# Kernel tuning notes

Measured on AMD Instinct MI355X. Metric: run time of the kernel, lower is better.

The kernel has to match this reference:

```python
import jax, jax.numpy as jnp
import numpy as np

NUM_EDGE_CLASS = 4
NODE_DIM = 64
BATCH = 8
NUM_NODES = 512


def setup_inputs() -> dict:
    key = jax.random.key(0)
    k1, k2, k3, k4, k5 = jax.random.split(key, 5)
    node_state = jax.random.normal(k1, (BATCH, NUM_NODES, NODE_DIM), dtype=jnp.float32)
    adj_mat = jax.random.randint(k2, (BATCH, NUM_NODES, NUM_NODES), 0, NUM_EDGE_CLASS, dtype=jnp.int32)
    matrix_in = jax.random.normal(k3, (NUM_EDGE_CLASS, NODE_DIM, NODE_DIM), dtype=jnp.float32) * 0.1
    matrix_out = jax.random.normal(k4, (NUM_EDGE_CLASS, NODE_DIM, NODE_DIM), dtype=jnp.float32) * 0.1
    bias = jax.random.normal(k5, (2 * NODE_DIM,), dtype=jnp.float32) * 0.1
    return {"node_state": node_state, "adj_mat": adj_mat,
            "matrix_in": matrix_in, "matrix_out": matrix_out, "bias": bias}


def reference(node_state, adj_mat, matrix_in, matrix_out, bias):
    # Original builds a_in[b,v,w] = matrix_in[adj[b,v,w]] ([B,N,N,D,D]) and a giant
    # [B, N*D, N*D] block matrix; equivalently, with one-hot over edge classes:
    #   msg_in[b,v,d]  = sum_w matrix_in[adj[b,v,w]][d,e]  * h[b,w,e]
    #   msg_out[b,v,d] = sum_w matrix_out[adj[b,w,v]][d,e] * h[b,w,e]  (transposed adj)
    oh = jax.nn.one_hot(adj_mat, matrix_in.shape[0], dtype=node_state.dtype)  # [B,V,W,C]
    msg_in = jnp.einsum('bvwc,cde,bwe->bvd', oh, matrix_in, node_state)
    msg_out = jnp.einsum('bwvc,cde,bwe->bvd', oh, matrix_out, node_state)
    return jnp.concatenate([msg_in, msg_out], axis=-1) + bias  # [B,N,2D]
```

## Files before the change

kernel.cpp:

```cpp
#include <hip/hip_runtime.h>

#define NB 8
#define NN 512
#define DD 64
#define NCLS 4

typedef short bf16x8 __attribute__((ext_vector_type(8)));
typedef float f32x4 __attribute__((ext_vector_type(4)));

__device__ __forceinline__ unsigned short f2bf(float f) {
    unsigned int x = __builtin_bit_cast(unsigned int, f);
    x += 0x7FFFu + ((x >> 16) & 1u);
    return (unsigned short)(x >> 16);
}

__device__ __forceinline__ void gload_lds16(const void* g, void* lds) {
    __builtin_amdgcn_global_load_lds(
        (const __attribute__((address_space(1))) unsigned int*)g,
        (__attribute__((address_space(3))) unsigned int*)lds, 16, 0, 0);
}

__device__ __forceinline__ bf16x8 onehot_packed(unsigned int bits, unsigned int cls) {
    union { unsigned int u[4]; bf16x8 v; } r;
    #pragma unroll
    for (int j = 0; j < 4; ++j) {
        unsigned int c0 = (bits >> (4 * j)) & 3u;
        unsigned int c1 = (bits >> (4 * j + 2)) & 3u;
        r.u[j] = (c0 == cls ? 0x3F80u : 0u) | (c1 == cls ? 0x3F800000u : 0u);
    }
    return r.v;
}

__global__ __launch_bounds__(256) void prep_kernel(
    const float* __restrict__ h, const int* __restrict__ adj,
    const float* __restrict__ Min, const float* __restrict__ Mout,
    unsigned int* __restrict__ packR, unsigned int* __restrict__ packC,
    unsigned short* __restrict__ HTbf, unsigned short* __restrict__ Wbf)
{
    const int blk = blockIdx.x, t = threadIdx.x;
    if (blk < 64) {
        const int b = blk >> 3, r0 = (blk & 7) * 64;
        #pragma unroll
        for (int i = 0; i < 8; ++i) {
            int idx = i * 256 + t;
            int row = r0 + (idx >> 5), pk = idx & 31;
            const int* src = adj + ((size_t)b * NN + row) * NN + pk * 16;
            unsigned int u = 0;
            #pragma unroll
            for (int j = 0; j < 16; ++j) u |= ((unsigned int)src[j] & 3u) << (2 * j);
            packR[((size_t)b * NN + row) * 32 + pk] = u;
        }
    } else if (blk < 576) {
        __shared__ int tile[64][65];
        __shared__ __align__(16) unsigned int tp[64][4];
        const int bb = blk - 64;
        const int b = bb >> 6, tr = ((bb >> 3) & 7) * 64, tc = (bb & 7) * 64;
        const int* src = adj + (size_t)b * NN * NN;
        #pragma unroll
        for (int i = 0; i < 16; ++i) {
            int idx = i * 256 + t, rr = idx >> 6, cc = idx & 63;
            tile[rr][cc] = src[(size_t)(tr + rr) * NN + tc + cc];
        }
        __syncthreads();
        {
            int row = t & 63, part = t >> 6;
            unsigned int u = 0;
            #pragma unroll
            for (int j = 0; j < 16; ++j)
                u |= ((unsigned int)tile[part * 16 + j][row] & 3u) << (2 * j);
            tp[row][part] = u;
        }
        __syncthreads();
        if (t < 64)
            *(uint4*)&packC[((size_t)b * NN + tc + t) * 32 + (tr >> 4)] =
                *(const uint4*)&tp[t][0];
    } else if (blk < 640) {
        const int bb = blk - 576;
        #pragma unroll
        for (int i = 0; i < 16; ++i) {
            int idx = bb * 4096 + i * 256 + t;
            int w = idx & 511, e = (idx >> 9) & 63, b = idx >> 15;
            HTbf[((size_t)b * DD + e) * NN + w] = f2bf(h[((size_t)b * NN + w) * DD + e]);
        }
    } else {
        int idx = (blk - 640) * 256 + t;
        int dir = idx >> 14, d = (idx >> 8) & 63, k = idx & 255;
        int c = k >> 6, e = k & 63;
        const float* M = dir ? Mout : Min;
        Wbf[idx] = f2bf(M[(c * DD + d) * DD + e]);
    }
}

__global__ __launch_bounds__(256) void msg_mfma_kernel(
    const unsigned int* __restrict__ packR, const unsigned int* __restrict__ packC,
    const unsigned short* __restrict__ HTbf, const unsigned short* __restrict__ Wbf,
    const float* __restrict__ bias, float* __restrict__ out)
{
    __shared__ unsigned short HT[2][DD][128];
    __shared__ unsigned short S2[2][8][NCLS * DD];

    const int t = threadIdx.x;
    const int lane = t & 63, wv = t >> 6;
    const int dir = wv >> 1, rt = wv & 1;
    const int b = blockIdx.x >> 6;
    const int v0 = (blockIdx.x & 63) * 8;
    const int r = lane & 15, kb = lane >> 4;

    const unsigned short* HTg = HTbf + (size_t)b * DD * NN;

    auto stage = [&](int s, int c0) {
        #pragma unroll
        for (int q = 0; q < 4; ++q) {
            int L = wv * 4 + q;
            int e = 4 * L + (lane >> 4);
            int off = ((lane & 15) << 4) ^ ((e & 7) << 4);
            const unsigned short* src = HTg + e * NN + c0 * 128 + (off >> 1);
            gload_lds16(src, &HT[s][4 * L][0]);
        }
    };

    stage(0, 0);

    const int vloc = rt * 4 + (r >> 2);
    const unsigned int cls = (unsigned int)(r & 3);
    const unsigned short* prow = (const unsigned short*)(
        (dir ? packC : packR) + ((size_t)b * NN + v0 + vloc) * 32);
    unsigned int bits0  = prow[kb];        unsigned int bits1  = prow[4 + kb];
    unsigned int bits2  = prow[8 + kb];    unsigned int bits3  = prow[12 + kb];
    unsigned int bits4  = prow[16 + kb];   unsigned int bits5  = prow[20 + kb];
    unsigned int bits6  = prow[24 + kb];   unsigned int bits7  = prow[28 + kb];
    unsigned int bits8  = prow[32 + kb];   unsigned int bits9  = prow[36 + kb];
    unsigned int bits10 = prow[40 + kb];   unsigned int bits11 = prow[44 + kb];
    unsigned int bits12 = prow[48 + kb];   unsigned int bits13 = prow[52 + kb];
    unsigned int bits14 = prow[56 + kb];   unsigned int bits15 = prow[60 + kb];

    __syncthreads();

    f32x4 acc[4] = {f32x4{0,0,0,0}, f32x4{0,0,0,0}, f32x4{0,0,0,0}, f32x4{0,0,0,0}};
    #pragma unroll
    for (int c = 0; c < 4; ++c) {
        int s = c & 1;
        if (c < 3) stage(s ^ 1, c + 1);
        #pragma unroll
        for (int kc = 0; kc < 4; ++kc) {
            unsigned int bits;
            switch (c * 4 + kc) {
                case 0:  bits = bits0;  break;  case 1:  bits = bits1;  break;
                case 2:  bits = bits2;  break;  case 3:  bits = bits3;  break;
                case 4:  bits = bits4;  break;  case 5:  bits = bits5;  break;
                case 6:  bits = bits6;  break;  case 7:  bits = bits7;  break;
                case 8:  bits = bits8;  break;  case 9:  bits = bits9;  break;
                case 10: bits = bits10; break;  case 11: bits = bits11; break;
                case 12: bits = bits12; break;  case 13: bits = bits13; break;
                case 14: bits = bits14; break;  default: bits = bits15; break;
            }
            bf16x8 afrag = onehot_packed(bits, cls);
            #pragma unroll
            for (int n = 0; n < 4; ++n) {
                int e = n * 16 + r;
                int boff = (kc * 64 + (kb << 4)) ^ ((e & 7) << 4);
                bf16x8 bfrag = *(const bf16x8*)((const char*)&HT[s][e][0] + boff);
                acc[n] = __builtin_amdgcn_mfma_f32_16x16x32_bf16(afrag, bfrag, acc[n], 0, 0, 0);
            }
        }
        __syncthreads();
    }

    #pragma unroll
    for (int ct = 0; ct < 4; ++ct) {
        #pragma unroll
        for (int rg = 0; rg < 4; ++rg) {
            int row_g = rt * 16 + kb * 4 + rg;
            int vv = row_g >> 2, cc2 = row_g & 3;
            int e = ct * 16 + r;
            int rb = (cc2 * 128 + e * 2) ^ ((vv & 7) << 4);
            *(unsigned short*)((char*)&S2[dir][vv][0] + rb) = f2bf(acc[ct][rg]);
        }
    }
    __syncthreads();

    f32x4 acc2[2] = {f32x4{0,0,0,0}, f32x4{0,0,0,0}};
    #pragma unroll
    for (int kc = 0; kc < 8; ++kc) {
        int vv = r & 7;
        int kbase = kc * 32 + kb * 8;
        int rb = (kbase * 2) ^ (vv << 4);
        bf16x8 a2 = *(const bf16x8*)((const char*)&S2[dir][vv][0] + rb);
        #pragma unroll
        for (int j = 0; j < 2; ++j) {
            int d = (rt * 2 + j) * 16 + r;
            bf16x8 b2 = *(const bf16x8*)&Wbf[(dir * DD + d) * 256 + kbase];
            acc2[j] = __builtin_amdgcn_mfma_f32_16x16x32_bf16(a2, b2, acc2[j], 0, 0, 0);
        }
    }
    #pragma unroll
    for (int j = 0; j < 2; ++j) {
        int d = (rt * 2 + j) * 16 + r;
        float bs = bias[dir * DD + d];
        #pragma unroll
        for (int rg = 0; rg < 4; ++rg) {
            int row = kb * 4 + rg;
            if (row < 8)
                out[((size_t)(b * NN + v0 + row)) * (2 * DD) + dir * DD + d] = acc2[j][rg] + bs;
        }
    }
}

__global__ __launch_bounds__(256) void msg_kernel(
    const float* __restrict__ h, const int* __restrict__ adj,
    const float* __restrict__ Min, const float* __restrict__ Mout,
    const float* __restrict__ bias, float* __restrict__ out)
{
    __shared__ __align__(16) float S[4][2][NCLS][DD];
    const int lane = threadIdx.x & 63, wslot = threadIdx.x >> 6;
    const int wid = blockIdx.x * 4 + wslot;
    const int b = wid >> 9, v = wid & (NN - 1);
    const float* hb = h + (size_t)b * NN * DD;
    const int* adjb = adj + (size_t)b * NN * NN;
    float tot = 0.f, ain1 = 0.f, ain2 = 0.f, ain3 = 0.f, aout1 = 0.f, aout2 = 0.f, aout3 = 0.f;
    for (int w0 = 0; w0 < NN; w0 += 64) {
        int cin_chunk = adjb[v * NN + (w0 + lane)];
        int cout_chunk = adjb[(w0 + lane) * NN + v];
        #pragma unroll
        for (int k = 0; k < 64; ++k) {
            float hw = hb[(w0 + k) * DD + lane];
            int cin = __builtin_amdgcn_readlane(cin_chunk, k);
            int cout = __builtin_amdgcn_readlane(cout_chunk, k);
            tot += hw;
            ain1 = fmaf((cin == 1) ? 1.f : 0.f, hw, ain1);
            ain2 = fmaf((cin == 2) ? 1.f : 0.f, hw, ain2);
            ain3 = fmaf((cin == 3) ? 1.f : 0.f, hw, ain3);
            aout1 = fmaf((cout == 1) ? 1.f : 0.f, hw, aout1);
            aout2 = fmaf((cout == 2) ? 1.f : 0.f, hw, aout2);
            aout3 = fmaf((cout == 3) ? 1.f : 0.f, hw, aout3);
        }
    }
    S[wslot][0][0][lane] = tot - ain1 - ain2 - ain3;
    S[wslot][0][1][lane] = ain1; S[wslot][0][2][lane] = ain2; S[wslot][0][3][lane] = ain3;
    S[wslot][1][0][lane] = tot - aout1 - aout2 - aout3;
    S[wslot][1][1][lane] = aout1; S[wslot][1][2][lane] = aout2; S[wslot][1][3][lane] = aout3;
    __syncthreads();
    float o_in = 0.f, o_out = 0.f;
    #pragma unroll
    for (int c = 0; c < NCLS; ++c)
        for (int e0 = 0; e0 < DD; e0 += 4) {
            float4 mi = *reinterpret_cast<const float4*>(&Min[(c * DD + lane) * DD + e0]);
            float4 mo = *reinterpret_cast<const float4*>(&Mout[(c * DD + lane) * DD + e0]);
            float4 si = *reinterpret_cast<const float4*>(&S[wslot][0][c][e0]);
            float4 so = *reinterpret_cast<const float4*>(&S[wslot][1][c][e0]);
            o_in = fmaf(mi.x, si.x, fmaf(mi.y, si.y, fmaf(mi.z, si.z, fmaf(mi.w, si.w, o_in))));
            o_out = fmaf(mo.x, so.x, fmaf(mo.y, so.y, fmaf(mo.z, so.z, fmaf(mo.w, so.w, o_out))));
        }
    float* ov = out + (size_t)(b * NN + v) * (2 * DD);
    ov[lane] = o_in + bias[lane];
    ov[DD + lane] = o_out + bias[DD + lane];
}

extern "C" void kernel_launch(void* const* d_in, const int* in_sizes, int n_in,
                              void* d_out, int out_size, void* d_ws, size_t ws_size,
                              hipStream_t stream) {
    const float* node_state = (const float*)d_in[0];
    const int*   adj_mat    = (const int*)  d_in[1];
    const float* matrix_in  = (const float*)d_in[2];
    const float* matrix_out = (const float*)d_in[3];
    const float* bias       = (const float*)d_in[4];
    float* out = (float*)d_out;

    const size_t PACKR_OFF = 0;
    const size_t PACKC_OFF = (size_t)NB * NN * 32 * 4;
    const size_t HT_OFF    = PACKC_OFF + (size_t)NB * NN * 32 * 4;
    const size_t W_OFF     = HT_OFF + (size_t)NB * DD * NN * 2;
    const size_t NEED      = W_OFF + (size_t)2 * DD * 256 * 2;

    if (ws_size < NEED) {
        msg_kernel<<<NB * NN / 4, 256, 0, stream>>>(node_state, adj_mat, matrix_in,
                                                    matrix_out, bias, out);
        return;
    }
    unsigned int*   packR = (unsigned int*)((char*)d_ws + PACKR_OFF);
    unsigned int*   packC = (unsigned int*)((char*)d_ws + PACKC_OFF);
    unsigned short* HTbf  = (unsigned short*)((char*)d_ws + HT_OFF);
    unsigned short* Wbf   = (unsigned short*)((char*)d_ws + W_OFF);

    prep_kernel<<<768, 256, 0, stream>>>(node_state, adj_mat, matrix_in, matrix_out,
                                         packR, packC, HTbf, Wbf);
    msg_mfma_kernel<<<NB * NN / 8, 256, 0, stream>>>(packR, packC, HTbf, Wbf, bias, out);
}
```

Measured before the change: 22.05 us.

## Fuse row and column adjacency packing, tile node transpose via LDS, SWAR one-hot

The prep kernel now reads each 64x64 adjacency tile once and emits both the row-packed and column-packed 2-bit codes from it, so the separate row-pack blocks and their second full read of the adjacency matrix go away. The node-state transpose to bf16 is staged through a padded LDS tile so global reads and writes are coalesced, with writes packed two bf16 values at a time. The one-hot fragment builder uses an XOR/OR bitmask trick against a replicated class pattern, replacing per-element compares. Total prep grid shrinks and the fused blocks do more work each, which may lengthen the critical block.

```diff
diff --git a/kernel.cpp b/kernel.cpp
--- a/kernel.cpp
+++ b/kernel.cpp
@@ -20,13 +20,15 @@
         (__attribute__((address_space(3))) unsigned int*)lds, 16, 0, 0);
 }
 
-__device__ __forceinline__ bf16x8 onehot_packed(unsigned int bits, unsigned int cls) {
+__device__ __forceinline__ bf16x8 onehot_packed(unsigned int bits, unsigned int rep) {
+    unsigned int x = bits ^ rep;
+    unsigned int y = x | (x >> 1);
+    unsigned int m = ~y & 0x55555555u;
     union { unsigned int u[4]; bf16x8 v; } r;
     #pragma unroll
     for (int j = 0; j < 4; ++j) {
-        unsigned int c0 = (bits >> (4 * j)) & 3u;
-        unsigned int c1 = (bits >> (4 * j + 2)) & 3u;
-        r.u[j] = (c0 == cls ? 0x3F80u : 0u) | (c1 == cls ? 0x3F800000u : 0u);
+        unsigned int f = m >> (4 * j);
+        r.u[j] = ((f & 1u) ? 0x3F80u : 0u) | ((f & 4u) ? 0x3F800000u : 0u);
     }
     return r.v;
 }
@@ -38,23 +40,10 @@
     unsigned short* __restrict__ HTbf, unsigned short* __restrict__ Wbf)
 {
     const int blk = blockIdx.x, t = threadIdx.x;
-    if (blk < 64) {
-        const int b = blk >> 3, r0 = (blk & 7) * 64;
-        #pragma unroll
-        for (int i = 0; i < 8; ++i) {
-            int idx = i * 256 + t;
-            int row = r0 + (idx >> 5), pk = idx & 31;
-            const int* src = adj + ((size_t)b * NN + row) * NN + pk * 16;
-            unsigned int u = 0;
-            #pragma unroll
-            for (int j = 0; j < 16; ++j) u |= ((unsigned int)src[j] & 3u) << (2 * j);
-            packR[((size_t)b * NN + row) * 32 + pk] = u;
-        }
-    } else if (blk < 576) {
+    if (blk < 512) {
         __shared__ int tile[64][65];
-        __shared__ __align__(16) unsigned int tp[64][4];
-        const int bb = blk - 64;
-        const int b = bb >> 6, tr = ((bb >> 3) & 7) * 64, tc = (bb & 7) * 64;
+        const int b = blk >> 6, ti = blk & 63;
+        const int tr = (ti >> 3) * 64, tc = (ti & 7) * 64;
         const int* src = adj + (size_t)b * NN * NN;
         #pragma unroll
         for (int i = 0; i < 16; ++i) {
@@ -63,27 +52,35 @@
         }
         __syncthreads();
         {
-            int row = t & 63, part = t >> 6;
-            unsigned int u = 0;
+            int r = t >> 2, g = t & 3;
+            unsigned int ur = 0, uc = 0;
             #pragma unroll
-            for (int j = 0; j < 16; ++j)
-                u |= ((unsigned int)tile[part * 16 + j][row] & 3u) << (2 * j);
-            tp[row][part] = u;
+            for (int j = 0; j < 16; ++j) {
+                ur |= ((unsigned int)tile[r][16 * g + j] & 3u) << (2 * j);
+                uc |= ((unsigned int)tile[16 * g + j][r] & 3u) << (2 * j);
+            }
+            packR[((size_t)b * NN + tr + r) * 32 + (tc >> 4) + g] = ur;
+            packC[((size_t)b * NN + tc + r) * 32 + (tr >> 4) + g] = uc;
+        }
+    } else if (blk < 576) {
+        __shared__ float tf[64][65];
+        const int bb = blk - 512, b = bb >> 3, w0 = (bb & 7) * 64;
+        #pragma unroll
+        for (int i = 0; i < 16; ++i) {
+            int idx = i * 256 + t, w = idx >> 6, e = idx & 63;
+            tf[w][e] = h[((size_t)b * NN + w0 + w) * DD + e];
         }
         __syncthreads();
-        if (t < 64)
-            *(uint4*)&packC[((size_t)b * NN + tc + t) * 32 + (tr >> 4)] =
-                *(const uint4*)&tp[t][0];
-    } else if (blk < 640) {
-        const int bb = blk - 576;
-        #pragma unroll
-        for (int i = 0; i < 16; ++i) {
-            int idx = bb * 4096 + i * 256 + t;
-            int w = idx & 511, e = (idx >> 9) & 63, b = idx >> 15;
-            HTbf[((size_t)b * DD + e) * NN + w] = f2bf(h[((size_t)b * NN + w) * DD + e]);
+        #pragma unroll
+        for (int i = 0; i < 8; ++i) {
+            int e = 8 * i + (t >> 5), wl = t & 31;
+            unsigned int lo = f2bf(tf[2 * wl][e]);
+            unsigned int hi = f2bf(tf[2 * wl + 1][e]);
+            *(unsigned int*)&HTbf[((size_t)b * DD + e) * NN + w0 + 2 * wl] =
+                lo | (hi << 16);
         }
     } else {
-        int idx = (blk - 640) * 256 + t;
+        int idx = (blk - 576) * 256 + t;
         int dir = idx >> 14, d = (idx >> 8) & 63, k = idx & 255;
         int c = k >> 6, e = k & 63;
         const float* M = dir ? Mout : Min;
@@ -122,7 +119,7 @@
     stage(0, 0);
 
     const int vloc = rt * 4 + (r >> 2);
-    const unsigned int cls = (unsigned int)(r & 3);
+    const unsigned int rep = (unsigned int)(r & 3) * 0x55555555u;
     const unsigned short* prow = (const unsigned short*)(
         (dir ? packC : packR) + ((size_t)b * NN + v0 + vloc) * 32);
     unsigned int bits0  = prow[kb];        unsigned int bits1  = prow[4 + kb];
@@ -154,7 +151,7 @@
                 case 12: bits = bits12; break;  case 13: bits = bits13; break;
                 case 14: bits = bits14; break;  default: bits = bits15; break;
             }
-            bf16x8 afrag = onehot_packed(bits, cls);
+            bf16x8 afrag = onehot_packed(bits, rep);
             #pragma unroll
             for (int n = 0; n < 4; ++n) {
                 int e = n * 16 + r;
@@ -282,7 +279,7 @@
     unsigned short* HTbf  = (unsigned short*)((char*)d_ws + HT_OFF);
     unsigned short* Wbf   = (unsigned short*)((char*)d_ws + W_OFF);
 
-    prep_kernel<<<768, 256, 0, stream>>>(node_state, adj_mat, matrix_in, matrix_out,
+    prep_kernel<<<704, 256, 0, stream>>>(node_state, adj_mat, matrix_in, matrix_out,
                                          packR, packC, HTbf, Wbf);
     msg_mfma_kernel<<<NB * NN / 8, 256, 0, stream>>>(packR, packC, HTbf, Wbf, bias, out);
 }
```

Measured after the change: 21.11 us. -4.3%, faster.
